# Kernel tuning notes

Hardware: AMD Instinct MI355X
Metric: run time of the kernel (lower is better)

The kernel has to match this reference:

```python
import jax, jax.numpy as jnp
import numpy as np
import math

# dims (match init_kwargs / input_specs)
T, B, S = 2048, 8, 512
D, H, DFF, NQ, W = 512, 8, 2048, 10, 16
EPS = 1e-5
NEG = -1e30


def _ln(x, g, b):
    mu = jnp.mean(x, axis=-1, keepdims=True)
    var = jnp.mean((x - mu) ** 2, axis=-1, keepdims=True)
    return (x - mu) * jax.lax.rsqrt(var + EPS) * g + b


def setup_inputs() -> dict:
    key = jax.random.key(0)
    ks = jax.random.split(key, 10)
    f = lambda k, shape, s=0.02: jax.random.normal(k, shape, jnp.float32) * s
    return {
        'tgt': jax.random.normal(ks[0], (T, B, D), jnp.float32),
        'memory': jax.random.normal(ks[1], (S, B, D), jnp.float32),
        'queries': f(ks[2], (NQ, D), 1.0 / math.sqrt(D)),
        'wk': f(ks[3], (NQ, 1), 1.0 / math.sqrt(NQ)),
        'in_proj_w': f(ks[4], (3 * D, D)),
        'in_proj_b': jnp.zeros((3 * D,), jnp.float32),
        'out_proj_w': f(ks[5], (D, D)),
        'out_proj_b': jnp.zeros((D,), jnp.float32),
        'lin1_w': f(ks[6], (DFF, D)),
        'lin1_b': jnp.zeros((DFF,), jnp.float32),
        'lin2_w': f(ks[7], (D, DFF)),
        'lin2_b': jnp.zeros((D,), jnp.float32),
        'ln1_g': jnp.ones((D,), jnp.float32), 'ln1_b': jnp.zeros((D,), jnp.float32),
        'ln2_g': jnp.ones((D,), jnp.float32), 'ln2_b': jnp.zeros((D,), jnp.float32),
        'ln3_g': jnp.ones((D,), jnp.float32), 'ln3_b': jnp.zeros((D,), jnp.float32),
    }


def _qa_block(x, queries, wk):
    # x: (T, B, D). Learned queries: per-head unit-norm + depth scale (QaN).
    dh = D // H
    q = queries.reshape(NQ, H, dh)
    q = q / (jnp.linalg.norm(q, axis=-1, keepdims=True) + 1e-6)
    q = (q / math.sqrt(dh)).reshape(NQ, D)
    # LocalAttention(window=W, look_backward=1, look_forward=1, non-causal, autopad)
    # k = v = x; T % W == 0 so autopad is a no-op.
    xb = jnp.transpose(x, (1, 0, 2))                       # (B, T, D)
    nw = T // W
    scale = D ** -0.5                                      # dim_head = D (single-head local attn)
    bk = xb.reshape(B, nw, W, D)
    pad = jnp.zeros((B, 1, W, D), x.dtype)
    bkp = jnp.concatenate([pad, bk, pad], axis=1)          # (B, nw+2, W, D)
    kv = jnp.concatenate([bkp[:, i:i + nw] for i in range(3)], axis=2)  # (B, nw, 3W, D)
    win_ok = jnp.pad(jnp.ones((nw,), bool), (1, 1))
    vm = jnp.stack([win_ok[i:i + nw] for i in range(3)], axis=1)        # (nw, 3)
    kmask = jnp.repeat(vm, W, axis=1)                                   # (nw, 3W)
    # The query vector is identical for every time step, so every position in a
    # window sees the same (query, keyset) pair -> one attention row per (n, window).
    sim = jnp.einsum('nd,bmjd->bnmj', q * scale, kv)       # (B, NQ, nw, 3W)
    sim = jnp.where(kmask[None, None], sim, NEG)
    attn = jax.nn.softmax(sim, axis=-1)
    out = jnp.einsum('bnmj,bmjd->bnmd', attn, kv)          # (B, NQ, nw, D)
    out = jnp.einsum('bnmd,n->bmd', out, wk[:, 0])         # mix N queries via wk (N,1)
    out = jnp.broadcast_to(out[:, :, None], (B, nw, W, D)).reshape(B, T, D)
    return jnp.transpose(out, (1, 0, 2))                   # (T, B, D)


def _mha_block(x, mem, in_w, in_b, out_w, out_b):
    dh = D // H
    wq, wkk, wv = jnp.split(in_w, 3, axis=0)
    bq, bk, bv = jnp.split(in_b, 3)
    q = (x @ wq.T + bq).reshape(T, B, H, dh).transpose(1, 2, 0, 3)   # (B,H,T,dh)
    k = (mem @ wkk.T + bk).reshape(S, B, H, dh).transpose(1, 2, 0, 3)
    v = (mem @ wv.T + bv).reshape(S, B, H, dh).transpose(1, 2, 0, 3)
    attn = jax.nn.softmax(jnp.einsum('bhtd,bhsd->bhts', q, k) / math.sqrt(dh), axis=-1)
    o = jnp.einsum('bhts,bhsd->bhtd', attn, v).transpose(2, 0, 1, 3).reshape(T, B, D)
    return o @ out_w.T + out_b


def reference(tgt, memory, queries, wk, in_proj_w, in_proj_b, out_proj_w, out_proj_b,
              lin1_w, lin1_b, lin2_w, lin2_b, ln1_g, ln1_b, ln2_g, ln2_b, ln3_g, ln3_b):
    # post-norm (norm_first=False), eval mode: dropouts + stochastic_depth(rate=0) are identity
    x = tgt
    x = _ln(x + _qa_block(x, queries, wk), ln1_g, ln1_b)
    x = _ln(x + _mha_block(x, memory, in_proj_w, in_proj_b, out_proj_w, out_proj_b), ln2_g, ln2_b)
    ff = jax.nn.relu(x @ lin1_w.T + lin1_b) @ lin2_w.T + lin2_b
    x = _ln(x + ff, ln3_g, ln3_b)
    # x = tgt + stochastic_depth(x - tgt) == x in eval / rate 0
    return x
```

## Files before the change

### kernel.cpp

```cpp
#include <hip/hip_runtime.h>


typedef unsigned short u16;
typedef unsigned int u32;
typedef short short8_t __attribute__((ext_vector_type(8)));
typedef float f32x4 __attribute__((ext_vector_type(4)));

#define TT 2048
#define BB 8
#define SS 512
#define DD 512
#define HH 8
#define DH 64
#define DFF 2048
#define NQ 10
#define WW 16
#define NW 128
#define KVPART 2097152

__device__ __forceinline__ float b2f(u16 u) {
    return __uint_as_float(((unsigned int)u) << 16);
}
__device__ __forceinline__ u16 f2b(float f) {
    unsigned int x = __float_as_uint(f);
    unsigned int r = x + 0x7FFFu + ((x >> 16) & 1u);
    return (u16)(r >> 16);
}
__device__ __forceinline__ u32 cvt_pk_bf16(float lo, float hi) {
    u32 r;
    asm volatile("v_cvt_pk_bf16_f32 %0, %1, %2" : "=v"(r) : "v"(lo), "v"(hi));
    return r;
}
__device__ __forceinline__ float wave_sum(float v) {
    #pragma unroll
    for (int o = 32; o > 0; o >>= 1) v += __shfl_xor(v, o, 64);
    return v;
}
__device__ __forceinline__ float wave_max(float v) {
    #pragma unroll
    for (int o = 32; o > 0; o >>= 1) v = fmaxf(v, __shfl_xor(v, o, 64));
    return v;
}
__device__ __forceinline__ void load4(const u16* p, float* v) {
    ushort4 t = *(const ushort4*)p;
    v[0] = b2f(t.x); v[1] = b2f(t.y); v[2] = b2f(t.z); v[3] = b2f(t.w);
}
__device__ __forceinline__ void load4(const float* p, float* v) {
    float4 t = *(const float4*)p;
    v[0] = t.x; v[1] = t.y; v[2] = t.z; v[3] = t.w;
}
__device__ __forceinline__ void st1(u16* p, float v) { *p = f2b(v); }
__device__ __forceinline__ void st1(float* p, float v) { *p = v; }

__device__ __forceinline__ void async16(const u16* g, u16* l) {
    __builtin_amdgcn_global_load_lds((const __attribute__((address_space(1))) u32*)g,
                                     (__attribute__((address_space(3))) u32*)l, 16, 0, 0);
}

__device__ __forceinline__ void xcd_remap(int& bx, int& by) {
    int flat = blockIdx.y * gridDim.x + blockIdx.x;
    int xcd = flat & 7;
    int j = flat >> 3;
    by = xcd * ((int)gridDim.y >> 3) + j / (int)gridDim.x;
    bx = j % (int)gridDim.x;
}

__device__ __forceinline__ void cvt_block(const float* s, u16* d, int base) {
    int i = base + threadIdx.x * 4;
    float4 v = *(const float4*)(s + i);
    ushort4 o;
    o.x = f2b(v.x); o.y = f2b(v.y); o.z = f2b(v.z); o.w = f2b(v.w);
    *(ushort4*)(d + i) = o;
}

__global__ __launch_bounds__(256) void cvt2_kernel(const float* __restrict__ s0,
                                                   const float* __restrict__ s1,
                                                   u16* __restrict__ d0,
                                                   u16* __restrict__ d1) {
    int bid = blockIdx.x;
    if (bid < 2048) cvt_block(s0, d0, bid * 1024);
    else            cvt_block(s1, d1, (bid - 2048) * 1024);
}

__global__ __launch_bounds__(256) void cvt3_kernel(const float* __restrict__ s0,
                                                   const float* __restrict__ s1,
                                                   const float* __restrict__ s2,
                                                   u16* __restrict__ d0,
                                                   u16* __restrict__ d1,
                                                   u16* __restrict__ d2) {
    int bid = blockIdx.x;
    if (bid < 256) {
        cvt_block(s0, d0, bid * 1024);
    } else if (bid < 1280) {
        cvt_block(s1, d1, (bid - 256) * 1024);
    } else {
        int g = (bid - 1280) * 256 + threadIdx.x;
        int l = g & 63, ot = (g >> 6) & 31, c = g >> 11;
        int quad = l >> 4;
        int o = ot * 16 + (l & 15);
        const float* src = s2 + (size_t)o * DFF + c * 32 + 4 * quad;
        float4 v0 = *(const float4*)(src);
        float4 v1 = *(const float4*)(src + 16);
        ushort4 o0, o1;
        o0.x = f2b(v0.x); o0.y = f2b(v0.y); o0.z = f2b(v0.z); o0.w = f2b(v0.w);
        o1.x = f2b(v1.x); o1.y = f2b(v1.y); o1.z = f2b(v1.z); o1.w = f2b(v1.w);
        u16* dst = d2 + (size_t)g * 8;
        *(ushort4*)(dst) = o0;
        *(ushort4*)(dst + 4) = o1;
    }
}

__global__ __launch_bounds__(512) void qeff_kernel(const float* __restrict__ queries,
                                                   float* __restrict__ qeff) {
    int d = threadIdx.x;
    const float KS = 0.0055242717280199026f;
    for (int n = 0; n < NQ; n++) {
        float v = queries[n * DD + d];
        float ss = wave_sum(v * v);
        float norm = sqrtf(ss);
        qeff[n * DD + d] = v / (norm + 1e-6f) * KS;
    }
}

__global__ __launch_bounds__(256) void p_kernel(const float* __restrict__ x,
                                                const float* __restrict__ qeff,
                                                float* __restrict__ p) {
    __shared__ float qe[NQ * DD];
    for (int i = threadIdx.x; i < NQ * DD; i += 256) qe[i] = qeff[i];
    __syncthreads();
    int b = blockIdx.x >> 9;
    int t = ((blockIdx.x & 511) << 2) + (threadIdx.x >> 6);
    int lane = threadIdx.x & 63;
    const float* xr = x + ((size_t)t * BB + b) * DD;
    float acc[NQ];
    #pragma unroll
    for (int n = 0; n < NQ; n++) acc[n] = 0.f;
    #pragma unroll
    for (int c = 0; c < 8; c++) {
        int d = c * 64 + lane;
        float xv = xr[d];
        #pragma unroll
        for (int n = 0; n < NQ; n++) acc[n] += xv * qe[n * DD + d];
    }
    #pragma unroll
    for (int n = 0; n < NQ; n++) {
        float s = wave_sum(acc[n]);
        if (lane == 0) p[((size_t)(b * NQ + n)) * TT + t] = s;
    }
}

__global__ __launch_bounds__(256) void winmix_kernel(const float* __restrict__ p,
                                                     const float* __restrict__ wk,
                                                     const float* __restrict__ x,
                                                     float* __restrict__ mixed) {
    __shared__ float As[48];
    int id = blockIdx.x;
    int b = id >> 7, m = id & 127;
    if (threadIdx.x < 64) {
        int j = threadIdx.x;
        int tj = (m - 1) * WW + j;
        bool valid = (j < 48) && (tj >= 0) && (tj < TT);
        float acc = 0.f;
        for (int n = 0; n < NQ; n++) {
            float v = valid ? p[((size_t)(b * NQ + n)) * TT + tj] : -1e30f;
            float mx = wave_max(v);
            float e = valid ? __expf(v - mx) : 0.f;
            float s = wave_sum(e);
            acc += wk[n] * (e / s);
        }
        if (j < 48) As[j] = acc;
    }
    __syncthreads();
    int d0 = threadIdx.x, d1 = threadIdx.x + 256;
    float a0 = 0.f, a1 = 0.f;
    int tb = (m - 1) * WW;
    for (int j = 0; j < 48; j++) {
        int t = tb + j;
        if ((unsigned)t < (unsigned)TT) {
            float aj = As[j];
            const float* xr = x + ((size_t)t * BB + b) * DD;
            a0 += aj * xr[d0];
            a1 += aj * xr[d1];
        }
    }
    mixed[(size_t)id * DD + d0] = a0;
    mixed[(size_t)id * DD + d1] = a1;
}

__global__ __launch_bounds__(256) void ln_qa_kernel(const float* __restrict__ a,
                                                    const float* __restrict__ mixed,
                                                    const float* __restrict__ g,
                                                    const float* __restrict__ bt,
                                                    u16* __restrict__ out) {
    int r = blockIdx.x * 4 + (threadIdx.x >> 6);
    int lane = threadIdx.x & 63;
    int t = r >> 3, b = r & 7;
    const float* ar = a + (size_t)r * DD;
    const float* mr = mixed + ((size_t)(b * NW + (t >> 4))) * DD;
    int d0 = lane * 8;
    float av[8], mv[8], gg[8], bb[8];
    load4(ar + d0, av); load4(ar + d0 + 4, av + 4);
    load4(mr + d0, mv); load4(mr + d0 + 4, mv + 4);
    load4(g + d0, gg);  load4(g + d0 + 4, gg + 4);
    load4(bt + d0, bb); load4(bt + d0 + 4, bb + 4);
    float v[8];
    float s = 0.f, s2 = 0.f;
    #pragma unroll
    for (int u = 0; u < 8; u++) { v[u] = av[u] + mv[u]; s += v[u]; s2 += v[u] * v[u]; }
    s = wave_sum(s); s2 = wave_sum(s2);
    float mu = s * (1.f / DD);
    float var = s2 * (1.f / DD) - mu * mu;
    float rs = rsqrtf(var + 1e-5f);
    #pragma unroll
    for (int u = 0; u < 8; u++) out[(size_t)r * DD + d0 + u] = f2b((v[u] - mu) * rs * gg[u] + bb[u]);
}

template <typename OT>
__global__ __launch_bounds__(256) void ln_rows_kernel(const u16* __restrict__ a,
                                                      const u16* __restrict__ bsrc,
                                                      const float* __restrict__ g,
                                                      const float* __restrict__ bt,
                                                      OT* __restrict__ out) {
    int r = blockIdx.x * 4 + (threadIdx.x >> 6);
    int lane = threadIdx.x & 63;
    const u16* ar = a + (size_t)r * DD;
    const u16* br = bsrc + (size_t)r * DD;
    int d0 = lane * 8;
    float av[8], cv[8], gg[8], bb[8];
    load4(ar + d0, av); load4(ar + d0 + 4, av + 4);
    load4(br + d0, cv); load4(br + d0 + 4, cv + 4);
    load4(g + d0, gg);  load4(g + d0 + 4, gg + 4);
    load4(bt + d0, bb); load4(bt + d0 + 4, bb + 4);
    float v[8];
    float s = 0.f, s2 = 0.f;
    #pragma unroll
    for (int u = 0; u < 8; u++) { v[u] = av[u] + cv[u]; s += v[u]; s2 += v[u] * v[u]; }
    s = wave_sum(s); s2 = wave_sum(s2);
    float mu = s * (1.f / DD);
    float var = s2 * (1.f / DD) - mu * mu;
    float rs = rsqrtf(var + 1e-5f);
    #pragma unroll
    for (int u = 0; u < 8; u++) st1(out + (size_t)r * DD + d0 + u, (v[u] - mu) * rs * gg[u] + bb[u]);
}

template <int RELU, int MT, int KV>
__global__ __launch_bounds__(256) void gemm_lds(const u16* __restrict__ A,
                                                const u16* __restrict__ W,
                                                const float* __restrict__ bias,
                                                u16* __restrict__ C,
                                                int M, int N, int K) {
    constexpr int BM = MT * 32;
    constexpr int NIA = BM / 64;
    __shared__ u16 As[2][BM * 32];
    __shared__ u16 Bs[2][128 * 32];
    int tid = threadIdx.x;
    int w = tid >> 6, lane = tid & 63;
    int n16 = lane & 15, quad = lane >> 4;
    int m0 = blockIdx.y * BM, n0 = blockIdx.x * 128;
    int wm16 = (w >> 1) * MT;
    int wn = (w & 1) * 64;

    const u16* gA[NIA];
    u16* lA[NIA];
    #pragma unroll
    for (int i = 0; i < NIA; i++) {
        int s = (w * NIA + i) * 64 + lane;
        int mb = s >> 6, kseg = (s >> 4) & 3, m = s & 15;
        gA[i] = A + (size_t)(m0 + mb * 16 + m) * K + kseg * 8;
        lA[i] = &As[0][(size_t)((w * NIA + i) * 64) * 8];
    }
    const u16* gB[2];
    u16* lB[2];
    #pragma unroll
    for (int i = 0; i < 2; i++) {
        int s = (w * 2 + i) * 64 + lane;
        int nb = s >> 6, kseg = (s >> 4) & 3, n = s & 15;
        gB[i] = W + (size_t)(n0 + nb * 16 + n) * K + kseg * 8;
        lB[i] = &Bs[0][(size_t)((w * 2 + i) * 64) * 8];
    }

    f32x4 acc[MT][4];
    #pragma unroll
    for (int i = 0; i < MT; i++)
        #pragma unroll
        for (int j = 0; j < 4; j++) acc[i][j] = (f32x4){0.f, 0.f, 0.f, 0.f};

    const int nk = K >> 5;
    #pragma unroll
    for (int i = 0; i < NIA; i++) async16(gA[i], lA[i]);
    #pragma unroll
    for (int i = 0; i < 2; i++) async16(gB[i], lB[i]);
    __syncthreads();

    for (int t = 0; t < nk; t++) {
        int cur = t & 1;
        if (t + 1 < nk) {
            int nxt = cur ^ 1;
            #pragma unroll
            for (int i = 0; i < NIA; i++) async16(gA[i] + (t + 1) * 32, lA[i] + nxt * (BM * 32));
            #pragma unroll
            for (int i = 0; i < 2; i++) async16(gB[i] + (t + 1) * 32, lB[i] + nxt * 4096);
        }
        const u16* Ac = &As[cur][0];
        const u16* Bc = &Bs[cur][0];
        short8_t af[MT], bf[4];
        #pragma unroll
        for (int im = 0; im < MT; im++)
            af[im] = *(const short8_t*)(Ac + (size_t)((wm16 + im) * 64 + lane) * 8);
        #pragma unroll
        for (int in = 0; in < 4; in++)
            bf[in] = *(const short8_t*)(Bc + (size_t)(((w & 1) * 4 + in) * 64 + lane) * 8);
        #pragma unroll
        for (int im = 0; im < MT; im++)
            #pragma unroll
            for (int in = 0; in < 4; in++)
                acc[im][in] = __builtin_amdgcn_mfma_f32_16x16x32_bf16(af[im], bf[in], acc[im][in], 0, 0, 0);
        __syncthreads();
    }

    float bia[4];
    #pragma unroll
    for (int in = 0; in < 4; in++) bia[in] = bias[n0 + wn + in * 16 + n16];
    #pragma unroll
    for (int im = 0; im < MT; im++) {
        #pragma unroll
        for (int r = 0; r < 4; r++) {
            int row = m0 + (wm16 + im) * 16 + quad * 4 + r;
            #pragma unroll
            for (int in = 0; in < 4; in++) {
                float v = acc[im][in][r] + bia[in];
                if (RELU) v = fmaxf(v, 0.f);
                if (KV) {
                    int col = n0 + wn + in * 16 + n16;
                    int part = col >> 9, h = (col >> 6) & 7, d = col & 63;
                    int s = row >> 3, bq = row & 7;
                    C[(size_t)part * KVPART + ((size_t)(bq * HH + h) * SS + s) * DH + d] = f2b(v);
                } else {
                    C[(size_t)row * N + n0 + wn + in * 16 + n16] = f2b(v);
                }
            }
        }
    }
}

template <int RELU, int KV>
__global__ __launch_bounds__(256) void gemm_np(const u16* __restrict__ A,
                                               const u16* __restrict__ W,
                                               const float* __restrict__ bias,
                                               u16* __restrict__ C,
                                               int M, int N, int K) {
    __shared__ u16 As[3][64 * 32];
    __shared__ u16 Bs[3][64 * 32];
    int tid = threadIdx.x;
    int w = tid >> 6, lane = tid & 63;
    int n16 = lane & 15, quad = lane >> 4;
    int bx, by;
    xcd_remap(bx, by);
    int m0 = by * 64, n0 = bx * 64;
    int wm16 = (w >> 1) * 2;
    int wn = (w & 1) * 32;

    const u16* gA0 = A + (size_t)(m0 + w * 16 + n16) * K + quad * 8;
    const u16* gB0 = W + (size_t)(n0 + w * 16 + n16) * K + quad * 8;

    f32x4 acc[2][2];
    #pragma unroll
    for (int i = 0; i < 2; i++)
        #pragma unroll
        for (int j = 0; j < 2; j++) acc[i][j] = (f32x4){0.f, 0.f, 0.f, 0.f};

    const int nk = K >> 5;
    async16(gA0, &As[0][w * 512]);
    async16(gB0, &Bs[0][w * 512]);
    async16(gA0 + 32, &As[1][w * 512]);
    async16(gB0 + 32, &Bs[1][w * 512]);

    int cur = 0;
    for (int t = 0; t < nk; t++) {
        if (t + 1 < nk) {
            __asm__ volatile("s_waitcnt vmcnt(2)" ::: "memory");
        } else {
            __asm__ volatile("s_waitcnt vmcnt(0)" ::: "memory");
        }
        __builtin_amdgcn_s_barrier();
        __builtin_amdgcn_sched_barrier(0);
        if (t + 2 < nk) {
            int nx2 = cur + 2; if (nx2 >= 3) nx2 -= 3;
            async16(gA0 + (t + 2) * 32, &As[nx2][w * 512]);
            async16(gB0 + (t + 2) * 32, &Bs[nx2][w * 512]);
        }
        const u16* Ac = &As[cur][0];
        const u16* Bc = &Bs[cur][0];
        short8_t af[2], bf[2];
        #pragma unroll
        for (int im = 0; im < 2; im++)
            af[im] = *(const short8_t*)(Ac + (size_t)((wm16 + im) * 64 + lane) * 8);
        #pragma unroll
        for (int in = 0; in < 2; in++)
            bf[in] = *(const short8_t*)(Bc + (size_t)(((w & 1) * 2 + in) * 64 + lane) * 8);
        #pragma unroll
        for (int im = 0; im < 2; im++)
            #pragma unroll
            for (int in = 0; in < 2; in++)
                acc[im][in] = __builtin_amdgcn_mfma_f32_16x16x32_bf16(af[im], bf[in], acc[im][in], 0, 0, 0);
        __asm__ volatile("s_waitcnt lgkmcnt(0)" ::: "memory");
        cur = (cur == 2) ? 0 : cur + 1;
    }

    float bia[2];
    #pragma unroll
    for (int in = 0; in < 2; in++) bia[in] = bias[n0 + wn + in * 16 + n16];
    #pragma unroll
    for (int im = 0; im < 2; im++) {
        #pragma unroll
        for (int r = 0; r < 4; r++) {
            int row = m0 + (wm16 + im) * 16 + quad * 4 + r;
            #pragma unroll
            for (int in = 0; in < 2; in++) {
                float v = acc[im][in][r] + bia[in];
                if (RELU) v = fmaxf(v, 0.f);
                if (KV) {
                    int col = n0 + wn + in * 16 + n16;
                    int part = col >> 9, h = (col >> 6) & 7, d = col & 63;
                    int s = row >> 3, bq = row & 7;
                    C[(size_t)part * KVPART + ((size_t)(bq * HH + h) * SS + s) * DH + d] = f2b(v);
                } else {
                    C[(size_t)row * N + n0 + wn + in * 16 + n16] = f2b(v);
                }
            }
        }
    }
}

__global__ __launch_bounds__(256, 2) void ffn_fused(const u16* __restrict__ A,
                                                    const u16* __restrict__ W1,
                                                    const float* __restrict__ b1,
                                                    const u16* __restrict__ W2s,
                                                    const float* __restrict__ b2,
                                                    u16* __restrict__ Cout) {
    __shared__ u16 W1b[2][32 * 512];
    __shared__ float b1s[DFF];
    int tid = threadIdx.x;
    int w = tid >> 6, lane = tid & 63;
    int n16 = lane & 15, quad = lane >> 4, q8 = quad * 8;
    int og = blockIdx.x;
    int m0 = blockIdx.y * 64;
    int row = m0 + w * 16 + n16;

    for (int i = tid; i < DFF; i += 256) b1s[i] = b1[i];

    short8_t aq[16];
    {
        const u16* ar = A + (size_t)row * DD + q8;
        #pragma unroll
        for (int ks = 0; ks < 16; ks++)
            aq[ks] = *(const short8_t*)(ar + ks * 32);
    }

    const u16* gW1 = W1 + (size_t)((w >> 1) * 16 + n16) * DD + ((w & 1) * 8) * 32 + q8;
    const u16* gW2 = W2s + (size_t)(og * 16) * 512 + lane * 8;

    f32x4 acc[16];
    #pragma unroll
    for (int ot = 0; ot < 16; ot++) acc[ot] = (f32x4){0.f, 0.f, 0.f, 0.f};

    union PU { u32 wd[4]; short8_t s8; };

    #pragma unroll
    for (int i = 0; i < 8; i++)
        async16(gW1 + i * 32, &W1b[0][(size_t)(w * 8 + i) * 512]);
    __syncthreads();

    for (int c = 0; c < 64; c++) {
        int cur = c & 1, nxt = cur ^ 1;

        short8_t w2f[16];
        {
            const u16* gw2c = gW2 + (size_t)c * 16384;
            #pragma unroll
            for (int f = 0; f < 16; f++)
                w2f[f] = *(const short8_t*)(gw2c + f * 512);
        }

        if (c < 63) {
            const u16* gW1c = gW1 + (size_t)(c + 1) * 32 * DD;
            #pragma unroll
            for (int i = 0; i < 8; i++)
                async16(gW1c + i * 32, &W1b[nxt][(size_t)(w * 8 + i) * 512]);
            __asm__ volatile("s_waitcnt vmcnt(24)" ::: "memory");
        } else {
            __asm__ volatile("s_waitcnt vmcnt(16)" ::: "memory");
        }
        __builtin_amdgcn_sched_barrier(0);

        f32x4 s0a = (f32x4){0.f, 0.f, 0.f, 0.f};
        f32x4 s0b = (f32x4){0.f, 0.f, 0.f, 0.f};
        f32x4 s1a = (f32x4){0.f, 0.f, 0.f, 0.f};
        f32x4 s1b = (f32x4){0.f, 0.f, 0.f, 0.f};
        #pragma unroll
        for (int ks = 0; ks < 8; ks++) {
            short8_t f0 = *(const short8_t*)&W1b[cur][(size_t)ks * 512 + lane * 8];
            s0a = __builtin_amdgcn_mfma_f32_16x16x32_bf16(f0, aq[ks], s0a, 0, 0, 0);
        }
        #pragma unroll
        for (int ks = 8; ks < 16; ks++) {
            short8_t f0 = *(const short8_t*)&W1b[cur][(size_t)ks * 512 + lane * 8];
            s0b = __builtin_amdgcn_mfma_f32_16x16x32_bf16(f0, aq[ks], s0b, 0, 0, 0);
        }
        #pragma unroll
        for (int ks = 0; ks < 8; ks++) {
            short8_t f1 = *(const short8_t*)&W1b[cur][(size_t)(16 + ks) * 512 + lane * 8];
            s1a = __builtin_amdgcn_mfma_f32_16x16x32_bf16(f1, aq[ks], s1a, 0, 0, 0);
        }
        #pragma unroll
        for (int ks = 8; ks < 16; ks++) {
            short8_t f1 = *(const short8_t*)&W1b[cur][(size_t)(16 + ks) * 512 + lane * 8];
            s1b = __builtin_amdgcn_mfma_f32_16x16x32_bf16(f1, aq[ks], s1b, 0, 0, 0);
        }
        f32x4 s0 = s0a + s0b;
        f32x4 s1 = s1a + s1b;

        float p0 = fmaxf(s0[0] + b1s[c * 32 + quad * 4 + 0], 0.f);
        float p1 = fmaxf(s0[1] + b1s[c * 32 + quad * 4 + 1], 0.f);
        float p2 = fmaxf(s0[2] + b1s[c * 32 + quad * 4 + 2], 0.f);
        float p3 = fmaxf(s0[3] + b1s[c * 32 + quad * 4 + 3], 0.f);
        float p4 = fmaxf(s1[0] + b1s[c * 32 + 16 + quad * 4 + 0], 0.f);
        float p5 = fmaxf(s1[1] + b1s[c * 32 + 16 + quad * 4 + 1], 0.f);
        float p6 = fmaxf(s1[2] + b1s[c * 32 + 16 + quad * 4 + 2], 0.f);
        float p7 = fmaxf(s1[3] + b1s[c * 32 + 16 + quad * 4 + 3], 0.f);

        PU pu;
        pu.wd[0] = cvt_pk_bf16(p0, p1);
        pu.wd[1] = cvt_pk_bf16(p2, p3);
        pu.wd[2] = cvt_pk_bf16(p4, p5);
        pu.wd[3] = cvt_pk_bf16(p6, p7);

        #pragma unroll
        for (int ot = 0; ot < 16; ot++)
            acc[ot] = __builtin_amdgcn_mfma_f32_16x16x32_bf16(pu.s8, w2f[ot], acc[ot], 0, 0, 0);

        __builtin_amdgcn_s_barrier();
    }

    #pragma unroll
    for (int ot = 0; ot < 16; ot++) {
        int col = og * 256 + ot * 16 + n16;
        float bia = b2[col];
        #pragma unroll
        for (int r = 0; r < 4; r++) {
            int ro = m0 + w * 16 + quad * 4 + r;
            Cout[(size_t)ro * DD + col] = f2b(acc[ot][r] + bia);
        }
    }
}

__global__ __launch_bounds__(256) void attn_wp(const u16* __restrict__ qb,
                                               const u16* __restrict__ kvb,
                                               u16* __restrict__ ob) {
    __shared__ u16 Kb[2][2048];
    __shared__ u16 Vt[2][64][40];
    int tid = threadIdx.x;
    int w = tid >> 6, lane = tid & 63;
    int n16 = lane & 15, quad = lane >> 4, q8 = quad * 8;
    int xb, bh;
    xcd_remap(xb, bh);
    int b = bh >> 3, h = bh & 7;
    int q0 = xb * 128 + w * 32;

    short8_t aq[2][2];
    #pragma unroll
    for (int qt = 0; qt < 2; qt++) {
        const u16* qrow = qb + ((size_t)(q0 + qt * 16 + n16) * BB + b) * DD + h * DH;
        aq[qt][0] = *(const short8_t*)(qrow + q8);
        aq[qt][1] = *(const short8_t*)(qrow + 32 + q8);
    }

    const u16* kbase = kvb + (size_t)(b * HH + h) * (SS * DH);
    const u16* vbase = kvb + (size_t)KVPART + (size_t)(b * HH + h) * (SS * DH);

    const u16* gK = kbase + (size_t)((w >> 1) * 16 + n16) * DH + (w & 1) * 32 + q8;

    int m = lane & 15;
    int a2 = m >> 2, b2 = m & 3;
    int key0 = (b2 < 2) ? (4 * a2 + 2 * b2) : (16 + 4 * a2 + 2 * (b2 - 2));
    int kp2 = m * 2;
    int vd = w * 16 + quad * 4;
    const u16* gV = vbase + (size_t)key0 * DH + vd;

    float lsum[2] = {0.f, 0.f};
    f32x4 Oa[2][4];
    #pragma unroll
    for (int qt = 0; qt < 2; qt++)
        #pragma unroll
        for (int ot = 0; ot < 4; ot++) Oa[qt][ot] = (f32x4){0.f, 0.f, 0.f, 0.f};

    union VU { ushort4 q; u16 h[4]; };
    union PU { u32 wd[4]; short8_t s8; };

    {
        async16(gK, &Kb[0][w * 512]);
        VU va, vb2;
        va.q  = *(const ushort4*)(gV);
        vb2.q = *(const ushort4*)(gV + DH);
        #pragma unroll
        for (int u = 0; u < 4; u++)
            *(u32*)&Vt[0][vd + u][kp2] = (u32)va.h[u] | ((u32)vb2.h[u] << 16);
    }
    __syncthreads();

    for (int c = 0; c < 16; c++) {
        int cur = c & 1, nxt = cur ^ 1;

        VU va, vb2;
        if (c < 15) {
            const u16* gVc = gV + (size_t)(c + 1) * 32 * DH;
            va.q  = *(const ushort4*)(gVc);
            vb2.q = *(const ushort4*)(gVc + DH);
            async16(gK + (size_t)(c + 1) * 32 * DH, &Kb[nxt][w * 512]);
        }

        short8_t bk0 = *(const short8_t*)&Kb[cur][0 * 512 + lane * 8];
        short8_t bk1 = *(const short8_t*)&Kb[cur][1 * 512 + lane * 8];
        short8_t bk2 = *(const short8_t*)&Kb[cur][2 * 512 + lane * 8];
        short8_t bk3 = *(const short8_t*)&Kb[cur][3 * 512 + lane * 8];

        #pragma unroll
        for (int qt = 0; qt < 2; qt++) {
            f32x4 s0 = (f32x4){0.f, 0.f, 0.f, 0.f};
            s0 = __builtin_amdgcn_mfma_f32_16x16x32_bf16(bk0, aq[qt][0], s0, 0, 0, 0);
            s0 = __builtin_amdgcn_mfma_f32_16x16x32_bf16(bk1, aq[qt][1], s0, 0, 0, 0);
            f32x4 s1 = (f32x4){0.f, 0.f, 0.f, 0.f};
            s1 = __builtin_amdgcn_mfma_f32_16x16x32_bf16(bk2, aq[qt][0], s1, 0, 0, 0);
            s1 = __builtin_amdgcn_mfma_f32_16x16x32_bf16(bk3, aq[qt][1], s1, 0, 0, 0);

            float p0 = __expf(s0[0] * 0.125f - 8.0f);
            float p1 = __expf(s0[1] * 0.125f - 8.0f);
            float p2 = __expf(s0[2] * 0.125f - 8.0f);
            float p3 = __expf(s0[3] * 0.125f - 8.0f);
            float p4 = __expf(s1[0] * 0.125f - 8.0f);
            float p5 = __expf(s1[1] * 0.125f - 8.0f);
            float p6 = __expf(s1[2] * 0.125f - 8.0f);
            float p7 = __expf(s1[3] * 0.125f - 8.0f);
            lsum[qt] += ((p0 + p1) + (p2 + p3)) + ((p4 + p5) + (p6 + p7));

            PU pu;
            pu.wd[0] = cvt_pk_bf16(p0, p1);
            pu.wd[1] = cvt_pk_bf16(p2, p3);
            pu.wd[2] = cvt_pk_bf16(p4, p5);
            pu.wd[3] = cvt_pk_bf16(p6, p7);

            #pragma unroll
            for (int ot = 0; ot < 4; ot++) {
                short8_t bv = *(const short8_t*)&Vt[cur][ot * 16 + n16][q8];
                Oa[qt][ot] = __builtin_amdgcn_mfma_f32_16x16x32_bf16(pu.s8, bv, Oa[qt][ot], 0, 0, 0);
            }
        }

        if (c < 15) {
            #pragma unroll
            for (int u = 0; u < 4; u++)
                *(u32*)&Vt[nxt][vd + u][kp2] = (u32)va.h[u] | ((u32)vb2.h[u] << 16);
        }
        __syncthreads();
    }

    #pragma unroll
    for (int qt = 0; qt < 2; qt++) {
        float l = lsum[qt];
        l += __shfl_xor(l, 16, 64);
        l += __shfl_xor(l, 32, 64);
        #pragma unroll
        for (int r = 0; r < 4; r++) {
            float lq = __shfl(l, quad * 4 + r, 64);
            float inv = 1.f / lq;
            int t = q0 + qt * 16 + quad * 4 + r;
            u16* orow = ob + ((size_t)t * BB + b) * DD + h * DH + n16;
            #pragma unroll
            for (int ot = 0; ot < 4; ot++) orow[ot * 16] = f2b(Oa[qt][ot][r] * inv);
        }
    }
}

extern "C" void kernel_launch(void* const* d_in, const int* in_sizes, int n_in,
                              void* d_out, int out_size, void* d_ws, size_t ws_size,
                              hipStream_t stream) {
    const float* tgt       = (const float*)d_in[0];
    const float* memory    = (const float*)d_in[1];
    const float* queries   = (const float*)d_in[2];
    const float* wk        = (const float*)d_in[3];
    const float* in_proj_w = (const float*)d_in[4];
    const float* in_proj_b = (const float*)d_in[5];
    const float* out_proj_w= (const float*)d_in[6];
    const float* out_proj_b= (const float*)d_in[7];
    const float* lin1_w    = (const float*)d_in[8];
    const float* lin1_b    = (const float*)d_in[9];
    const float* lin2_w    = (const float*)d_in[10];
    const float* lin2_b    = (const float*)d_in[11];
    const float* ln1_g     = (const float*)d_in[12];
    const float* ln1_b     = (const float*)d_in[13];
    const float* ln2_g     = (const float*)d_in[14];
    const float* ln2_b     = (const float*)d_in[15];
    const float* ln3_g     = (const float*)d_in[16];
    const float* ln3_b     = (const float*)d_in[17];

    char* w = (char*)d_ws;
    float* qeff  = (float*)(w + 0);
    float* pbuf  = (float*)(w + 20480);
    float* mixed = (float*)(w + 872448);
    u16* y1  = (u16*)(w + 2969600);
    u16* qb  = (u16*)(w + 19746816);
    u16* kvb = (u16*)(w + 36524032);
    u16* ob  = (u16*)(w + 44912640);
    u16* ipwb = (u16*)(w + 44912640);
    u16* memb = (u16*)(w + 46485504);
    u16* opwb  = (u16*)(w + 36524032);
    u16* l1wb  = (u16*)(w + 37048320);
    u16* l2sig = (u16*)(w + 39145472);
    u16* t1 = qb;
    u16* y2 = ob;
    u16* fb = y1;

    cvt2_kernel<<<2816, 256, 0, stream>>>(memory, in_proj_w, memb, ipwb);

    qeff_kernel<<<1, 512, 0, stream>>>(queries, qeff);
    p_kernel<<<BB * (TT / 4), 256, 0, stream>>>(tgt, qeff, pbuf);
    winmix_kernel<<<BB * NW, 256, 0, stream>>>(pbuf, wk, tgt, mixed);
    ln_qa_kernel<<<(TT * BB) / 4, 256, 0, stream>>>(tgt, mixed, ln1_g, ln1_b, y1);

    gemm_lds<0, 4, 0><<<dim3(DD / 128, (TT * BB) / 128), 256, 0, stream>>>(y1, ipwb, in_proj_b, qb, TT * BB, DD, DD);
    gemm_np<0, 1><<<dim3(1024 / 64, (SS * BB) / 64), 256, 0, stream>>>(memb, ipwb + (size_t)DD * DD, in_proj_b + DD, kvb, SS * BB, 1024, DD);
    attn_wp<<<dim3(TT / 128, BB * HH), 256, 0, stream>>>(qb, kvb, ob);
    cvt3_kernel<<<1792, 256, 0, stream>>>(out_proj_w, lin1_w, lin2_w, opwb, l1wb, l2sig);
    gemm_lds<0, 4, 0><<<dim3(DD / 128, (TT * BB) / 128), 256, 0, stream>>>(ob, opwb, out_proj_b, t1, TT * BB, DD, DD);
    ln_rows_kernel<u16><<<(TT * BB) / 4, 256, 0, stream>>>(y1, t1, ln2_g, ln2_b, y2);

    ffn_fused<<<dim3(2, (TT * BB) / 64), 256, 0, stream>>>(y2, l1wb, lin1_b, l2sig, lin2_b, fb);
    ln_rows_kernel<float><<<(TT * BB) / 4, 256, 0, stream>>>(y2, fb, ln3_g, ln3_b, (float*)d_out);
}
```

Baseline: 473.9 us.

## Split FFN over DFF halves instead of output columns, sum partials in final LN

The fused FFN kernel now splits work across the two blocks per row tile by halving the DFF (hidden) dimension rather than the output columns. This removes the duplicated first GEMM, since each block previously recomputed all 2048 hidden units for its 256 output columns. Each block now accumulates all 512 output columns, writing one of two bf16 partial sums, and a new LayerNorm kernel adds both partials to the residual. The cost is doubled accumulator and W2 fragment registers (32 tiles), which may spill or reduce occupancy. It also drops the explicit vmcnt waits in favour of a full __syncthreads per iteration, and adds an extra partial buffer round trip plus bf16 rounding of the partials.

```diff
diff --git a/kernel.cpp b/kernel.cpp
--- a/kernel.cpp
+++ b/kernel.cpp
@@ -243,6 +243,36 @@
     for (int u = 0; u < 8; u++) st1(out + (size_t)r * DD + d0 + u, (v[u] - mu) * rs * gg[u] + bb[u]);
 }
 
+__global__ __launch_bounds__(256) void ln_rows3_kernel(const u16* __restrict__ a,
+                                                       const u16* __restrict__ c0,
+                                                       const u16* __restrict__ c1,
+                                                       const float* __restrict__ g,
+                                                       const float* __restrict__ bt,
+                                                       float* __restrict__ out) {
+    int r = blockIdx.x * 4 + (threadIdx.x >> 6);
+    int lane = threadIdx.x & 63;
+    const u16* ar = a + (size_t)r * DD;
+    const u16* b0 = c0 + (size_t)r * DD;
+    const u16* b1 = c1 + (size_t)r * DD;
+    int d0 = lane * 8;
+    float av[8], v0[8], v1[8], gg[8], bb[8];
+    load4(ar + d0, av); load4(ar + d0 + 4, av + 4);
+    load4(b0 + d0, v0); load4(b0 + d0 + 4, v0 + 4);
+    load4(b1 + d0, v1); load4(b1 + d0 + 4, v1 + 4);
+    load4(g + d0, gg);  load4(g + d0 + 4, gg + 4);
+    load4(bt + d0, bb); load4(bt + d0 + 4, bb + 4);
+    float v[8];
+    float s = 0.f, s2 = 0.f;
+    #pragma unroll
+    for (int u = 0; u < 8; u++) { v[u] = av[u] + v0[u] + v1[u]; s += v[u]; s2 += v[u] * v[u]; }
+    s = wave_sum(s); s2 = wave_sum(s2);
+    float mu = s * (1.f / DD);
+    float var = s2 * (1.f / DD) - mu * mu;
+    float rs = rsqrtf(var + 1e-5f);
+    #pragma unroll
+    for (int u = 0; u < 8; u++) out[(size_t)r * DD + d0 + u] = (v[u] - mu) * rs * gg[u] + bb[u];
+}
+
 template <int RELU, int MT, int KV>
 __global__ __launch_bounds__(256) void gemm_lds(const u16* __restrict__ A,
                                                 const u16* __restrict__ W,
@@ -437,7 +467,8 @@
                                                     const float* __restrict__ b1,
                                                     const u16* __restrict__ W2s,
                                                     const float* __restrict__ b2,
-                                                    u16* __restrict__ Cout) {
+                                                    u16* __restrict__ P0,
+                                                    u16* __restrict__ P1) {
     __shared__ u16 W1b[2][32 * 512];
     __shared__ float b1s[DFF];
     int tid = threadIdx.x;
@@ -446,6 +477,7 @@
     int og = blockIdx.x;
     int m0 = blockIdx.y * 64;
     int row = m0 + w * 16 + n16;
+    int c0 = og * 32;
 
     for (int i = tid; i < DFF; i += 256) b1s[i] = b1[i];
 
@@ -457,12 +489,13 @@
             aq[ks] = *(const short8_t*)(ar + ks * 32);
     }
 
-    const u16* gW1 = W1 + (size_t)((w >> 1) * 16 + n16) * DD + ((w & 1) * 8) * 32 + q8;
-    const u16* gW2 = W2s + (size_t)(og * 16) * 512 + lane * 8;
-
-    f32x4 acc[16];
-    #pragma unroll
-    for (int ot = 0; ot < 16; ot++) acc[ot] = (f32x4){0.f, 0.f, 0.f, 0.f};
+    const u16* gW1 = W1 + (size_t)c0 * 32 * DD
+                   + (size_t)((w >> 1) * 16 + n16) * DD + ((w & 1) * 8) * 32 + q8;
+    const u16* gW2 = W2s + (size_t)c0 * 16384 + lane * 8;
+
+    f32x4 acc[32];
+    #pragma unroll
+    for (int ot = 0; ot < 32; ot++) acc[ot] = (f32x4){0.f, 0.f, 0.f, 0.f};
 
     union PU { u32 wd[4]; short8_t s8; };
 
@@ -471,27 +504,24 @@
         async16(gW1 + i * 32, &W1b[0][(size_t)(w * 8 + i) * 512]);
     __syncthreads();
 
-    for (int c = 0; c < 64; c++) {
-        int cur = c & 1, nxt = cur ^ 1;
-
-        short8_t w2f[16];
+    for (int ci = 0; ci < 32; ci++) {
+        int c = c0 + ci;
+        int cur = ci & 1, nxt = cur ^ 1;
+
+        short8_t w2f[32];
         {
-            const u16* gw2c = gW2 + (size_t)c * 16384;
-            #pragma unroll
-            for (int f = 0; f < 16; f++)
+            const u16* gw2c = gW2 + (size_t)ci * 16384;
+            #pragma unroll
+            for (int f = 0; f < 32; f++)
                 w2f[f] = *(const short8_t*)(gw2c + f * 512);
         }
 
-        if (c < 63) {
-            const u16* gW1c = gW1 + (size_t)(c + 1) * 32 * DD;
+        if (ci < 31) {
+            const u16* gW1c = gW1 + (size_t)(ci + 1) * 32 * DD;
             #pragma unroll
             for (int i = 0; i < 8; i++)
                 async16(gW1c + i * 32, &W1b[nxt][(size_t)(w * 8 + i) * 512]);
-            __asm__ volatile("s_waitcnt vmcnt(24)" ::: "memory");
-        } else {
-            __asm__ volatile("s_waitcnt vmcnt(16)" ::: "memory");
-        }
-        __builtin_amdgcn_sched_barrier(0);
+        }
 
         f32x4 s0a = (f32x4){0.f, 0.f, 0.f, 0.f};
         f32x4 s0b = (f32x4){0.f, 0.f, 0.f, 0.f};
@@ -536,20 +566,20 @@
         pu.wd[3] = cvt_pk_bf16(p6, p7);
 
         #pragma unroll
-        for (int ot = 0; ot < 16; ot++)
+        for (int ot = 0; ot < 32; ot++)
             acc[ot] = __builtin_amdgcn_mfma_f32_16x16x32_bf16(pu.s8, w2f[ot], acc[ot], 0, 0, 0);
 
-        __builtin_amdgcn_s_barrier();
-    }
-
-    #pragma unroll
-    for (int ot = 0; ot < 16; ot++) {
-        int col = og * 256 + ot * 16 + n16;
-        float bia = b2[col];
+        __syncthreads();
+    }
+
+    u16* Pout = og ? P1 : P0;
+    #pragma unroll
+    for (int ot = 0; ot < 32; ot++) {
+        float bia = og ? 0.f : b2[ot * 16 + n16];
         #pragma unroll
         for (int r = 0; r < 4; r++) {
             int ro = m0 + w * 16 + quad * 4 + r;
-            Cout[(size_t)ro * DD + col] = f2b(acc[ot][r] + bia);
+            Pout[(size_t)ro * DD + ot * 16 + n16] = f2b(acc[ot][r] + bia);
         }
     }
 }
@@ -718,7 +748,8 @@
     u16* l2sig = (u16*)(w + 39145472);
     u16* t1 = qb;
     u16* y2 = ob;
-    u16* fb = y1;
+    u16* P0 = qb;
+    u16* P1 = y1;
 
     cvt2_kernel<<<2816, 256, 0, stream>>>(memory, in_proj_w, memb, ipwb);
 
@@ -734,6 +765,6 @@
     gemm_lds<0, 4, 0><<<dim3(DD / 128, (TT * BB) / 128), 256, 0, stream>>>(ob, opwb, out_proj_b, t1, TT * BB, DD, DD);
     ln_rows_kernel<u16><<<(TT * BB) / 4, 256, 0, stream>>>(y1, t1, ln2_g, ln2_b, y2);
 
-    ffn_fused<<<dim3(2, (TT * BB) / 64), 256, 0, stream>>>(y2, l1wb, lin1_b, l2sig, lin2_b, fb);
-    ln_rows_kernel<float><<<(TT * BB) / 4, 256, 0, stream>>>(y2, fb, ln3_g, ln3_b, (float*)d_out);
-}
+    ffn_fused<<<dim3(2, (TT * BB) / 64), 256, 0, stream>>>(y2, l1wb, lin1_b, l2sig, lin2_b, P0, P1);
+    ln_rows3_kernel<<<(TT * BB) / 4, 256, 0, stream>>>(y2, P0, P1, ln3_g, ln3_b, (float*)d_out);
+}
```

New measurement: 660.1 us. 1.39x slower.
